# Kernel tuning notes

Hardware: AMD Instinct MI355X
Metric: run time of the kernel (lower is better)

Reference implementation:

```python
import jax, jax.numpy as jnp
import numpy as np


def setup_inputs() -> dict:
    key = jax.random.key(0)
    prediction = jax.random.normal(key, (16, 4096), dtype=jnp.float32)
    return {"prediction": prediction}


def reference(prediction):
    # prediction: [B, N]
    B, N = prediction.shape
    ntriu_elem = jnp.asarray(N * (N - 1) / 2, dtype=prediction.dtype)
    # pairwise_diff[b, i, j] = pred[b, i] - pred[b, j]  -> [B, N, N]
    pairwise_diff = prediction[:, :, None] - prediction[:, None, :]
    # torch.triu keeps j >= i (upper triangle incl. diagonal; diag is zero anyway)
    triu_mask = jnp.triu(jnp.ones((N, N), dtype=bool))  # [N, N]
    triu = jnp.where(triu_mask, pairwise_diff, jnp.zeros((), dtype=prediction.dtype))
    avg_diff = jnp.abs(triu).sum(axis=-1) / ntriu_elem  # [B, N]
    return avg_diff.mean()
```

## Files before the change

### kernel.cpp

```cpp
#include <hip/hip_runtime.h>


#define NN      4096
#define THREADS 256
#define R       8
#define JSEG    128
#define UPB     48

__global__ __launch_bounds__(THREADS) void pairdist_part(
    const float* __restrict__ pred, float* __restrict__ partials)
{
    const int blk = blockIdx.x;
    const int b   = blk / UPB;
    const int u   = blk % UPB;

    const int   ih = (u < 32) ? 0 : 1;
    const int   jh = (u < 32) ? u : (u - 16);
    const float w  = (u >= 16 && u < 32) ? 1.0f : 0.5f;

    const float* __restrict__ row = pred + (size_t)b * NN;

    __shared__ float sj[JSEG];
    if (threadIdx.x < JSEG)
        sj[threadIdx.x] = row[jh * JSEG + threadIdx.x];

    float pi[R];
#pragma unroll
    for (int k = 0; k < R; ++k)
        pi[k] = row[ih * (THREADS * R) + k * THREADS + threadIdx.x];

    __syncthreads();

    float acc[R];
#pragma unroll
    for (int k = 0; k < R; ++k) acc[k] = 0.0f;

#pragma unroll 4
    for (int j = 0; j < JSEG; j += 4) {
        float4 jv = *reinterpret_cast<const float4*>(&sj[j]);
#pragma unroll
        for (int k = 0; k < R; ++k) {
            acc[k] += fabsf(pi[k] - jv.x);
            acc[k] += fabsf(pi[k] - jv.y);
            acc[k] += fabsf(pi[k] - jv.z);
            acc[k] += fabsf(pi[k] - jv.w);
        }
    }

    float s = 0.0f;
#pragma unroll
    for (int k = 0; k < R; ++k) s += acc[k];

#pragma unroll
    for (int off = 32; off > 0; off >>= 1)
        s += __shfl_down(s, off, 64);

    __shared__ float sw[THREADS / 64];
    if ((threadIdx.x & 63) == 0) sw[threadIdx.x >> 6] = s;
    __syncthreads();

    if (threadIdx.x == 0)
        partials[blk] = ((sw[0] + sw[1]) + (sw[2] + sw[3])) * w;
}

__global__ __launch_bounds__(64) void pairdist_fin(
    const float* __restrict__ partials, float* __restrict__ out, double scale)
{
    double s = 0.0;
#pragma unroll
    for (int c = 0; c < 3; ++c) {
        float4 v = *reinterpret_cast<const float4*>(
            &partials[c * 256 + threadIdx.x * 4]);
        s += ((double)v.x + (double)v.y) + ((double)v.z + (double)v.w);
    }
#pragma unroll
    for (int off = 32; off > 0; off >>= 1)
        s += __shfl_down(s, off, 64);
    if (threadIdx.x == 0) out[0] = (float)(s * scale);
}

extern "C" void kernel_launch(void* const* d_in, const int* in_sizes, int n_in,
                              void* d_out, int out_size, void* d_ws, size_t ws_size,
                              hipStream_t stream) {
    const float* pred = (const float*)d_in[0];
    const int total = in_sizes[0];
    const int B = total / NN;
    const int nblocks = B * UPB;

    float* partials = (float*)d_ws;

    pairdist_part<<<nblocks, THREADS, 0, stream>>>(pred, partials);

    const double ntriu = (double)NN * (double)(NN - 1) * 0.5;
    const double scale = 1.0 / (ntriu * (double)B * (double)NN);
    pairdist_fin<<<1, 64, 0, stream>>>(partials, (float*)d_out, scale);
}
```

Before: 19.46 us.

## Split pairwise work into per-wave triangular chunks to skip lower-triangle tiles

Work is reassigned so each wavefront handles a 256-row by 128-column tile, and tiles are enumerated over the upper triangle only, using 16 row chunks with diagonal tiles weighted by one half. This removes most of the redundant lower-triangle computation the old half-split scheme performed, and it raises the block count from 48 to 68 per batch row. The block-level shared reduction and barrier are replaced by per-wave partial writes. The final kernel now sums 4352 partials instead of 768. A while-loop decode of the tile index per wave adds a little setup cost.

```diff
diff --git a/kernel.cpp b/kernel.cpp
--- a/kernel.cpp
+++ b/kernel.cpp
@@ -3,64 +3,60 @@
 
 #define NN      4096
 #define THREADS 256
-#define R       8
+#define WAVES   4
+#define R       4
+#define CSZ     256
 #define JSEG    128
-#define UPB     48
+#define UPR     272
+#define BPR     68
 
 __global__ __launch_bounds__(THREADS) void pairdist_part(
     const float* __restrict__ pred, float* __restrict__ partials)
 {
-    const int blk = blockIdx.x;
-    const int b   = blk / UPB;
-    const int u   = blk % UPB;
+    const int lane = threadIdx.x & 63;
+    const int wid  = threadIdx.x >> 6;
+    const int b    = blockIdx.x / BPR;
+    int u = (blockIdx.x % BPR) * WAVES + wid;
 
-    const int   ih = (u < 32) ? 0 : 1;
-    const int   jh = (u < 32) ? u : (u - 16);
-    const float w  = (u >= 16 && u < 32) ? 1.0f : 0.5f;
+    int c = 0;
+    while (u >= 32 - 2 * c) { u -= 32 - 2 * c; ++c; }
+    const int   jh = 2 * c + u;
+    const float w  = (u < 2) ? 0.5f : 1.0f;
 
     const float* __restrict__ row = pred + (size_t)b * NN;
 
-    __shared__ float sj[JSEG];
-    if (threadIdx.x < JSEG)
-        sj[threadIdx.x] = row[jh * JSEG + threadIdx.x];
+    __shared__ float sj[WAVES][JSEG];
+    sj[wid][lane]      = row[jh * JSEG + lane];
+    sj[wid][64 + lane] = row[jh * JSEG + 64 + lane];
 
     float pi[R];
 #pragma unroll
     for (int k = 0; k < R; ++k)
-        pi[k] = row[ih * (THREADS * R) + k * THREADS + threadIdx.x];
+        pi[k] = row[c * CSZ + k * 64 + lane];
 
     __syncthreads();
 
-    float acc[R];
-#pragma unroll
-    for (int k = 0; k < R; ++k) acc[k] = 0.0f;
-
-#pragma unroll 4
+    float a0 = 0.f, a1 = 0.f, a2 = 0.f, a3 = 0.f;
+#pragma unroll 8
     for (int j = 0; j < JSEG; j += 4) {
-        float4 jv = *reinterpret_cast<const float4*>(&sj[j]);
-#pragma unroll
-        for (int k = 0; k < R; ++k) {
-            acc[k] += fabsf(pi[k] - jv.x);
-            acc[k] += fabsf(pi[k] - jv.y);
-            acc[k] += fabsf(pi[k] - jv.z);
-            acc[k] += fabsf(pi[k] - jv.w);
-        }
+        float4 jv = *reinterpret_cast<const float4*>(&sj[wid][j]);
+        a0 += fabsf(pi[0] - jv.x); a1 += fabsf(pi[1] - jv.x);
+        a2 += fabsf(pi[2] - jv.x); a3 += fabsf(pi[3] - jv.x);
+        a0 += fabsf(pi[0] - jv.y); a1 += fabsf(pi[1] - jv.y);
+        a2 += fabsf(pi[2] - jv.y); a3 += fabsf(pi[3] - jv.y);
+        a0 += fabsf(pi[0] - jv.z); a1 += fabsf(pi[1] - jv.z);
+        a2 += fabsf(pi[2] - jv.z); a3 += fabsf(pi[3] - jv.z);
+        a0 += fabsf(pi[0] - jv.w); a1 += fabsf(pi[1] - jv.w);
+        a2 += fabsf(pi[2] - jv.w); a3 += fabsf(pi[3] - jv.w);
     }
-
-    float s = 0.0f;
-#pragma unroll
-    for (int k = 0; k < R; ++k) s += acc[k];
+    float s = (a0 + a1) + (a2 + a3);
 
 #pragma unroll
     for (int off = 32; off > 0; off >>= 1)
         s += __shfl_down(s, off, 64);
 
-    __shared__ float sw[THREADS / 64];
-    if ((threadIdx.x & 63) == 0) sw[threadIdx.x >> 6] = s;
-    __syncthreads();
-
-    if (threadIdx.x == 0)
-        partials[blk] = ((sw[0] + sw[1]) + (sw[2] + sw[3])) * w;
+    if (lane == 0)
+        partials[blockIdx.x * WAVES + wid] = s * w;
 }
 
 __global__ __launch_bounds__(64) void pairdist_fin(
@@ -68,9 +64,9 @@
 {
     double s = 0.0;
 #pragma unroll
-    for (int c = 0; c < 3; ++c) {
+    for (int cc = 0; cc < 17; ++cc) {
         float4 v = *reinterpret_cast<const float4*>(
-            &partials[c * 256 + threadIdx.x * 4]);
+            &partials[(cc * 64 + threadIdx.x) * 4]);
         s += ((double)v.x + (double)v.y) + ((double)v.z + (double)v.w);
     }
 #pragma unroll
@@ -85,7 +81,7 @@
     const float* pred = (const float*)d_in[0];
     const int total = in_sizes[0];
     const int B = total / NN;
-    const int nblocks = B * UPB;
+    const int nblocks = B * BPR;
 
     float* partials = (float*)d_ws;
 
```

After: 18.16 us. 1.07x faster.

## Replace brute-force pairwise sum with segment sort plus merge-rank cross terms

Applied to the files above, without the earlier changes.

Swaps the O(N^2) all-pairs absolute-difference loop for an approach that bitonic-sorts 64-element segments inside a wavefront. Within-segment pair sums come from the rank-weighted sorted values, and cross-segment sums come from a prefix scan plus binary search of each element's rank in the other segment. This cuts arithmetic sharply but adds a third kernel launch, a round trip of the sorted data through global memory, and extra shuffle and LDS traffic with serial binary searches.

```diff
diff --git a/kernel.cpp b/kernel.cpp
--- a/kernel.cpp
+++ b/kernel.cpp
@@ -1,78 +1,111 @@
 #include <hip/hip_runtime.h>
 
 
-#define NN      4096
-#define THREADS 256
-#define R       8
-#define JSEG    128
-#define UPB     48
+#define NN   4096
+#define SEG  64
+#define SPR  64
+#define TPRW 2016
+#define WPRW 252
 
-__global__ __launch_bounds__(THREADS) void pairdist_part(
-    const float* __restrict__ pred, float* __restrict__ partials)
+__global__ __launch_bounds__(256) void k1_sortseg(
+    const float* __restrict__ pred, float* __restrict__ sorted,
+    float* __restrict__ part)
 {
-    const int blk = blockIdx.x;
-    const int b   = blk / UPB;
-    const int u   = blk % UPB;
+    const int lane = threadIdx.x & 63;
+    const int wid  = threadIdx.x >> 6;
+    const int g    = blockIdx.x * 4 + wid;
+    const int row  = g >> 6;
+    const int seg  = g & 63;
 
-    const int   ih = (u < 32) ? 0 : 1;
-    const int   jh = (u < 32) ? u : (u - 16);
-    const float w  = (u >= 16 && u < 32) ? 1.0f : 0.5f;
+    float v = pred[(row << 12) + (seg << 6) + lane];
 
-    const float* __restrict__ row = pred + (size_t)b * NN;
-
-    __shared__ float sj[JSEG];
-    if (threadIdx.x < JSEG)
-        sj[threadIdx.x] = row[jh * JSEG + threadIdx.x];
-
-    float pi[R];
 #pragma unroll
-    for (int k = 0; k < R; ++k)
-        pi[k] = row[ih * (THREADS * R) + k * THREADS + threadIdx.x];
-
-    __syncthreads();
-
-    float acc[R];
+    for (int k = 2; k <= 64; k <<= 1) {
 #pragma unroll
-    for (int k = 0; k < R; ++k) acc[k] = 0.0f;
-
-#pragma unroll 4
-    for (int j = 0; j < JSEG; j += 4) {
-        float4 jv = *reinterpret_cast<const float4*>(&sj[j]);
-#pragma unroll
-        for (int k = 0; k < R; ++k) {
-            acc[k] += fabsf(pi[k] - jv.x);
-            acc[k] += fabsf(pi[k] - jv.y);
-            acc[k] += fabsf(pi[k] - jv.z);
-            acc[k] += fabsf(pi[k] - jv.w);
+        for (int j = k >> 1; j >= 1; j >>= 1) {
+            float o = __shfl_xor(v, j, 64);
+            bool up = ((lane & k) == 0) || (k == 64);
+            bool hi = (lane & j) != 0;
+            v = (hi == up) ? fmaxf(v, o) : fminf(v, o);
         }
     }
 
-    float s = 0.0f;
+    sorted[(g << 6) + lane] = v;
+
+    float t = (float)(2 * lane - 63) * v;
 #pragma unroll
-    for (int k = 0; k < R; ++k) s += acc[k];
+    for (int off = 32; off > 0; off >>= 1)
+        t += __shfl_down(t, off, 64);
+    if (lane == 0) part[g] = t;
+}
+
+__global__ __launch_bounds__(256) void k2_cross(
+    const float* __restrict__ sorted, float* __restrict__ part)
+{
+    __shared__ float sb[4][SEG];
+    __shared__ float sp[4][SEG];
+    __shared__ float cw[4];
+
+    const int lane = threadIdx.x & 63;
+    const int wid  = threadIdx.x >> 6;
+    const int wg   = blockIdx.x * 4 + wid;
+    const int row  = wg / WPRW;
+    const int q0   = (wg % WPRW) * 8;
+
+    float acc = 0.0f;
+
+#pragma unroll 2
+    for (int it = 0; it < 8; ++it) {
+        const int t = q0 + it;
+        int s1, s2;
+        if (t < 1984) {
+            const int d = 1 + (t >> 6);
+            s1 = t & 63;
+            s2 = (s1 + d) & 63;
+        } else {
+            s1 = t - 1984;
+            s2 = s1 + 32;
+        }
+        const float a = sorted[(((size_t)row << 6) + s1) * SEG + lane];
+        const float b = sorted[(((size_t)row << 6) + s2) * SEG + lane];
+
+        float inc = b;
+#pragma unroll
+        for (int j = 1; j < 64; j <<= 1) {
+            float u = __shfl_up(inc, j, 64);
+            if (lane >= j) inc += u;
+        }
+        const float SB = __shfl(inc, 63, 64);
+        sb[wid][lane] = b;
+        sp[wid][lane] = inc - b;
+
+        int c = 0;
+#pragma unroll
+        for (int step = 32; step >= 1; step >>= 1)
+            if (sb[wid][c + step - 1] < a) c += step;
+        if (sb[wid][c] < a) ++c;
+
+        const float Pc = (c < 64) ? sp[wid][c] : SB;
+        acc += (2.0f * (float)c - 64.0f) * a + SB - 2.0f * Pc;
+    }
 
 #pragma unroll
     for (int off = 32; off > 0; off >>= 1)
-        s += __shfl_down(s, off, 64);
+        acc += __shfl_down(acc, off, 64);
 
-    __shared__ float sw[THREADS / 64];
-    if ((threadIdx.x & 63) == 0) sw[threadIdx.x >> 6] = s;
+    if (lane == 0) cw[wid] = acc;
     __syncthreads();
-
     if (threadIdx.x == 0)
-        partials[blk] = ((sw[0] + sw[1]) + (sw[2] + sw[3])) * w;
+        part[blockIdx.x] = (cw[0] + cw[1]) + (cw[2] + cw[3]);
 }
 
-__global__ __launch_bounds__(64) void pairdist_fin(
-    const float* __restrict__ partials, float* __restrict__ out, double scale)
+__global__ __launch_bounds__(64) void k3_fin(
+    const float* __restrict__ part, int npart,
+    float* __restrict__ out, double scale)
 {
     double s = 0.0;
-#pragma unroll
-    for (int c = 0; c < 3; ++c) {
-        float4 v = *reinterpret_cast<const float4*>(
-            &partials[c * 256 + threadIdx.x * 4]);
-        s += ((double)v.x + (double)v.y) + ((double)v.z + (double)v.w);
-    }
+    for (int i = threadIdx.x; i < npart; i += 64)
+        s += (double)part[i];
 #pragma unroll
     for (int off = 32; off > 0; off >>= 1)
         s += __shfl_down(s, off, 64);
@@ -85,13 +118,21 @@
     const float* pred = (const float*)d_in[0];
     const int total = in_sizes[0];
     const int B = total / NN;
-    const int nblocks = B * UPB;
 
-    float* partials = (float*)d_ws;
+    const int nseg     = B * SPR;
+    const int k1_blks  = nseg / 4;
+    const int k2_blks  = B * WPRW / 4;
+    const int npart    = nseg + k2_blks;
 
-    pairdist_part<<<nblocks, THREADS, 0, stream>>>(pred, partials);
+    float* sorted = (float*)d_ws;
+    float* part   = sorted + (size_t)nseg * SEG;
+    float* wpart  = part;
+    float* cpart  = part + nseg;
+
+    k1_sortseg<<<k1_blks, 256, 0, stream>>>(pred, sorted, wpart);
+    k2_cross  <<<k2_blks, 256, 0, stream>>>(sorted, cpart);
 
     const double ntriu = (double)NN * (double)(NN - 1) * 0.5;
     const double scale = 1.0 / (ntriu * (double)B * (double)NN);
-    pairdist_fin<<<1, 64, 0, stream>>>(partials, (float*)d_out, scale);
+    k3_fin<<<1, 64, 0, stream>>>(part, npart, (float*)d_out, scale);
 }
```

New measurement: 24.62 us. +26.5%, slower.
